# Kernel optimization log

Hardware: AMD Instinct MI355X
Metric: run time of the kernel (lower is better)

Reference implementation:

```python
import jax, jax.numpy as jnp
import numpy as np

B, N, PS = 8, 2048, 32
P = N // PS          # 64 patches
D, MLP, DEPTH, H, DH = 1024, 2048, 6, 8, 64
INNER = H * DH       # 512
K = 20
EPS = 1e-5


def setup_inputs() -> dict:
    key = jax.random.key(0)
    ks = jax.random.split(key, 16)
    r = lambda i, shape: jax.random.normal(ks[i], shape, dtype=jnp.float32) * 0.02
    return {
        "x": jax.random.normal(ks[0], (B, N, 3), dtype=jnp.float32),
        "x_pos_embed": r(1, (B, P + 1, D)),
        "w1": r(2, (64, 6)),   "g1": jnp.ones(64),  "b1": jnp.zeros(64),
        "w2": r(3, (64, 128)), "g2": jnp.ones(64),  "b2": jnp.zeros(64),
        "w3": r(4, (128, 128)),"g3": jnp.ones(128), "b3": jnp.zeros(128),
        "w4": r(5, (256, 256)),"g4": jnp.ones(256), "b4": jnp.zeros(256),
        "w5": r(6, (D, 512)),  "g5": jnp.ones(D),   "b5": jnp.zeros(D),
        "cls_token": r(7, (1, 1, D)),
        "ln1_g": jnp.ones((DEPTH, D)), "ln1_b": jnp.zeros((DEPTH, D)),
        "wqkv": r(8, (DEPTH, D, 3 * INNER)),
        "wout": r(9, (DEPTH, INNER, D)), "bout": jnp.zeros((DEPTH, D)),
        "ln2_g": jnp.ones((DEPTH, D)), "ln2_b": jnp.zeros((DEPTH, D)),
        "wff1": r(10, (DEPTH, D, MLP)), "bff1": jnp.zeros((DEPTH, MLP)),
        "wff2": r(11, (DEPTH, MLP, D)), "bff2": jnp.zeros((DEPTH, D)),
    }


def _knn(x, k):  # x: [B, C, N] -> neighbor idx [B, N, k]
    xx = jnp.sum(x * x, axis=1)                        # [B, N]
    inner = jnp.einsum('bcn,bcm->bnm', x, x)           # [B, N, N]
    dist = 2.0 * inner - xx[:, :, None] - xx[:, None, :]  # = -||xi-xj||^2
    return jax.lax.top_k(dist, k)[1]


def _graph_feature(x, k):  # x: [B, C, N] -> [B, N, k, 2C]
    idx = _knn(x, k)
    xt = jnp.transpose(x, (0, 2, 1))                   # [B, N, C]
    nbr = jax.vmap(lambda f, i: f[i])(xt, idx)         # gather: [B, N, k, C]
    ctr = jnp.broadcast_to(xt[:, :, None, :], nbr.shape)
    return jnp.concatenate([nbr - ctr, ctr], axis=-1)


def _leaky(v):
    return jnp.where(v >= 0, v, 0.2 * v)


def _edge_conv(x, w, g, b, k):  # EdgeConv block: graph feat -> 1x1 conv -> BN(train) -> lrelu -> max over k
    f = _graph_feature(x, k)                           # [B, N, k, 2C]
    y = jnp.einsum('bnkc,oc->bonk', f, w)              # [B, O, N, k]
    mu = jnp.mean(y, axis=(0, 2, 3), keepdims=True)
    var = jnp.var(y, axis=(0, 2, 3), keepdims=True)
    y = (y - mu) * jax.lax.rsqrt(var + EPS) * g[None, :, None, None] + b[None, :, None, None]
    return jnp.max(_leaky(y), axis=-1)                 # [B, O, N]


def _ln(x, g, b):
    mu = jnp.mean(x, axis=-1, keepdims=True)
    var = jnp.var(x, axis=-1, keepdims=True)
    return (x - mu) * jax.lax.rsqrt(var + EPS) * g + b


def reference(x, x_pos_embed, w1, g1, b1, w2, g2, b2, w3, g3, b3, w4, g4, b4,
              w5, g5, b5, cls_token, ln1_g, ln1_b, wqkv, wout, bout,
              ln2_g, ln2_b, wff1, bff1, wff2, bff2):
    scale = DH ** -0.5
    pts = jnp.transpose(x, (0, 2, 1))                  # [B, 3, N]
    x1 = _edge_conv(pts, w1, g1, b1, K)                # [B, 64, N]
    x2 = _edge_conv(x1, w2, g2, b2, K)                 # [B, 64, N]
    x3 = _edge_conv(x2, w3, g3, b3, K)                 # [B, 128, N]
    x4 = _edge_conv(x3, w4, g4, b4, K)                 # [B, 256, N]
    h = jnp.concatenate([x1, x2, x3, x4], axis=1)      # [B, 512, N]
    y = jnp.einsum('bcn,oc->bon', h, w5)               # conv5 1x1 -> [B, D, N]
    mu = jnp.mean(y, axis=(0, 2), keepdims=True)
    var = jnp.var(y, axis=(0, 2), keepdims=True)
    y = _leaky((y - mu) * jax.lax.rsqrt(var + EPS) * g5[None, :, None] + b5[None, :, None])
    # patch max-pool: 'b (p n) c -> (b p) n c' then max over n
    t = jnp.transpose(y, (0, 2, 1)).reshape(B * P, PS, D)
    t = jnp.max(t, axis=1).reshape(B, P, D)
    t = jnp.concatenate([jnp.broadcast_to(cls_token, (B, 1, D)), t], axis=1)  # [B, P+1, D]
    for i in range(DEPTH):
        t = t + x_pos_embed
        hn = _ln(t, ln1_g[i], ln1_b[i])
        qkv = (hn @ wqkv[i]).reshape(B, P + 1, 3, H, DH)
        q, k_, v = [jnp.transpose(qkv[:, :, j], (0, 2, 1, 3)) for j in range(3)]
        attn = jax.nn.softmax(jnp.einsum('bhld,bhmd->bhlm', q, k_) * scale, axis=-1)
        z = jnp.einsum('bhlm,bhmd->bhld', attn, v)
        z = jnp.transpose(z, (0, 2, 1, 3)).reshape(B, P + 1, INNER)
        t = t + z @ wout[i] + bout[i]
        hn = _ln(t, ln2_g[i], ln2_b[i])
        t = t + jax.nn.gelu(hn @ wff1[i] + bff1[i], approximate=False) @ wff2[i] + bff2[i]
    return t[:, 1:]                                    # [B, P, D]
```

## Files before the change

kernel.cpp:

```cpp
#include <hip/hip_runtime.h>
#include <math.h>

#define BB 8
#define NN 2048
#define PSZ 32
#define PP 64
#define DD 1024
#define MLPD 2048
#define DEPTH_ 6
#define HH 8
#define DHH 64
#define INNER_ 512
#define KK 20
#define TOK 65
#define EPSF 1e-5f

#define GEMM_ACC 1
#define GEMM_GELU 2
#define GEMM_OUTBF16 4

typedef __bf16 bf16_t;
typedef __attribute__((ext_vector_type(8))) __bf16 bf16x8;
typedef __attribute__((ext_vector_type(4))) float f32x4;

__global__ void transpose_x_kernel(const float* __restrict__ x, float* __restrict__ pts) {
    int gid = blockIdx.x * blockDim.x + threadIdx.x;
    if (gid >= BB * NN * 3) return;
    int c = gid % 3; int n = (gid / 3) % NN; int b = gid / (3 * NN);
    pts[(b * 3 + c) * NN + n] = x[gid];
}

__global__ void sqnorm_kernel(const float* __restrict__ x, int bs, int C, float* __restrict__ xx) {
    int gid = blockIdx.x * blockDim.x + threadIdx.x;
    if (gid >= BB * NN) return;
    int n = gid % NN; int b = gid / NN;
    const float* xp = x + b * bs + n;
    float s = 0.f;
    for (int c = 0; c < C; ++c) { float v = xp[c * NN]; s += v * v; }
    xx[gid] = s;
}

__global__ __launch_bounds__(256) void dist_kernel(const float* __restrict__ x, int bs, int C,
                                                   const float* __restrict__ xx, int b0,
                                                   float* __restrict__ dist) {
    __shared__ __align__(16) float smem[4224];
    float (*As)[132] = (float(*)[132])smem;
    float (*Bs)[132] = (float(*)[132])(smem + 16 * 132);
    float (*tb)[132] = (float(*)[132])smem;

    int q = blockIdx.x;
    int bi = 0, rem = q;
    while (rem >= (16 - bi)) { rem -= (16 - bi); ++bi; }
    int bj = bi + rem;

    int b = b0 + blockIdx.z;
    int n0 = bi * 128, m0 = bj * 128;
    int tid = threadIdx.x;
    int ty = tid >> 4, tx = tid & 15;
    float acc[2][2][4][4] = {};
    const float* xb = x + (long)b * bs;
    for (int k0 = 0; k0 < C; k0 += 16) {
        #pragma unroll
        for (int p = 0; p < 2; ++p) {
            int li = tid + p * 256;
            int i4 = li & 31;
            int kk = li >> 5;
            int c = k0 + kk;
            float4 va = make_float4(0.f, 0.f, 0.f, 0.f);
            float4 vb = va;
            if (c < C) {
                va = *(const float4*)&xb[(long)c * NN + n0 + i4 * 4];
                vb = *(const float4*)&xb[(long)c * NN + m0 + i4 * 4];
            }
            *(float4*)&As[kk][i4 * 4] = va;
            *(float4*)&Bs[kk][i4 * 4] = vb;
        }
        __syncthreads();
        #pragma unroll
        for (int kk = 0; kk < 16; ++kk) {
            float a[2][4], bv[2][4];
            *(float4*)a[0] = *(const float4*)&As[kk][ty * 4];
            *(float4*)a[1] = *(const float4*)&As[kk][64 + ty * 4];
            *(float4*)bv[0] = *(const float4*)&Bs[kk][tx * 4];
            *(float4*)bv[1] = *(const float4*)&Bs[kk][64 + tx * 4];
            #pragma unroll
            for (int ri = 0; ri < 2; ++ri)
                #pragma unroll
                for (int ci = 0; ci < 2; ++ci)
                    #pragma unroll
                    for (int i = 0; i < 4; ++i)
                        #pragma unroll
                        for (int j = 0; j < 4; ++j)
                            acc[ri][ci][i][j] += a[ri][i] * bv[ci][j];
        }
        __syncthreads();
    }
    float* db = dist + (long)blockIdx.z * NN * NN;
    const float* xxb = xx + b * NN;
    float xm[2][4];
    #pragma unroll
    for (int ci = 0; ci < 2; ++ci)
        #pragma unroll
        for (int j = 0; j < 4; ++j)
            xm[ci][j] = xxb[m0 + ci * 64 + tx * 4 + j];
    #pragma unroll
    for (int ri = 0; ri < 2; ++ri)
        #pragma unroll
        for (int i = 0; i < 4; ++i) {
            float xn = xxb[n0 + ri * 64 + ty * 4 + i];
            #pragma unroll
            for (int ci = 0; ci < 2; ++ci)
                #pragma unroll
                for (int j = 0; j < 4; ++j)
                    acc[ri][ci][i][j] = 2.f * acc[ri][ci][i][j] - xn - xm[ci][j];
        }
    #pragma unroll
    for (int ri = 0; ri < 2; ++ri)
        #pragma unroll
        for (int i = 0; i < 4; ++i) {
            int n = n0 + ri * 64 + ty * 4 + i;
            #pragma unroll
            for (int ci = 0; ci < 2; ++ci)
                *(float4*)&db[(long)n * NN + m0 + ci * 64 + tx * 4] = *(float4*)&acc[ri][ci][i][0];
        }
    if (bi != bj) {
        #pragma unroll
        for (int s = 0; s < 4; ++s) {
            __syncthreads();
            int ci = s >> 1;
            if ((tx >> 3) == (s & 1)) {
                #pragma unroll
                for (int ri = 0; ri < 2; ++ri)
                    #pragma unroll
                    for (int j = 0; j < 4; ++j) {
                        float4 v;
                        v.x = acc[ri][ci][0][j];
                        v.y = acc[ri][ci][1][j];
                        v.z = acc[ri][ci][2][j];
                        v.w = acc[ri][ci][3][j];
                        *(float4*)&tb[(tx & 7) * 4 + j][ri * 64 + ty * 4] = v;
                    }
            }
            __syncthreads();
            int r = tid >> 3;
            int c0 = (tid & 7) * 16;
            long orow = (long)(m0 + s * 32 + r) * NN + n0 + c0;
            #pragma unroll
            for (int c4 = 0; c4 < 4; ++c4)
                *(float4*)&db[orow + c4 * 4] = *(const float4*)&tb[r][c0 + c4 * 4];
        }
    }
}

__global__ __launch_bounds__(256) void topk_kernel(const float* __restrict__ dist, int b0,
                                                   int* __restrict__ idx) {
    __shared__ float cval[4][64];
    __shared__ int   cidx[4][64];
    int b = b0 + blockIdx.y;
    int wid = threadIdx.x >> 6, lane = threadIdx.x & 63;
    int n = blockIdx.x * 4 + wid;
    const float* row = dist + ((long)blockIdx.y * NN + n) * NN;
    float vals[32];
    #pragma unroll
    for (int s = 0; s < 32; ++s) vals[s] = row[s * 64 + lane];
    int* op = idx + ((long)b * NN + n) * KK;

    float lm = vals[0];
    #pragma unroll
    for (int s = 1; s < 32; ++s) lm = fmaxf(lm, vals[s]);

    float sv = lm;
    #pragma unroll
    for (int k = 2; k <= 64; k <<= 1) {
        #pragma unroll
        for (int j = k >> 1; j > 0; j >>= 1) {
            float pv = __shfl_xor(sv, j);
            bool lower = (lane & j) == 0;
            bool up = (lane & k) != 0;
            bool ownBetter = sv > pv;
            bool keepOwn = ownBetter ^ (lower == up);
            sv = keepOwn ? sv : pv;
        }
    }
    float t = __shfl(sv, 19);

    int base = 0;
    #pragma unroll
    for (int s = 0; s < 32; ++s) {
        bool q = vals[s] >= t;
        unsigned long long m = __ballot(q);
        int my = base + (int)__builtin_amdgcn_mbcnt_hi((unsigned)(m >> 32),
                         __builtin_amdgcn_mbcnt_lo((unsigned)m, 0u));
        if (q && my < 64) { cval[wid][my] = vals[s]; cidx[wid][my] = s * 64 + lane; }
        base += (int)__popcll(m);
    }
    __asm__ volatile("s_waitcnt lgkmcnt(0)" ::: "memory");

    if (base <= 64) {
        float v = (lane < base) ? cval[wid][lane] : -INFINITY;
        int   ii = (lane < base) ? cidx[wid][lane] : 0x7FFFFFFF;
        #pragma unroll
        for (int k = 2; k <= 64; k <<= 1) {
            #pragma unroll
            for (int j = k >> 1; j > 0; j >>= 1) {
                float pv = __shfl_xor(v, j);
                int   pi = __shfl_xor(ii, j);
                bool lower = (lane & j) == 0;
                bool up = (lane & k) != 0;
                bool ownBetter = (v > pv) || (v == pv && ii < pi);
                bool keepOwn = ownBetter ^ (lower == up);
                if (!keepOwn) { v = pv; ii = pi; }
            }
        }
        if (lane < KK) op[lane] = ii;
    } else {
        for (int kk = 0; kk < KK; ++kk) {
            float bv = vals[0]; int bsl = 0;
            #pragma unroll
            for (int s = 1; s < 32; ++s) if (vals[s] > bv) { bv = vals[s]; bsl = s; }
            int bm = bsl * 64 + lane;
            for (int off = 32; off; off >>= 1) {
                float ov = __shfl_xor(bv, off);
                int om = __shfl_xor(bm, off);
                if (ov > bv || (ov == bv && om < bm)) { bv = ov; bm = om; }
            }
            int wslot = bm >> 6, wlane = bm & 63;
            #pragma unroll
            for (int s = 0; s < 32; ++s)
                if (s == wslot) vals[s] = (lane == wlane) ? -INFINITY : vals[s];
            if (lane == 0) op[kk] = bm;
        }
    }
}

__global__ __launch_bounds__(256) void pq_kernel(const float* __restrict__ x, int bs, int C,
                                                 const float* __restrict__ w, int O,
                                                 float* __restrict__ p, float* __restrict__ q) {
    __shared__ float wT[256][33];
    __shared__ float xs[128][32];
    int b = blockIdx.z;
    int o0 = blockIdx.y * 32;
    int n0 = blockIdx.x * 32;
    int tid = threadIdx.x;
    for (int i = tid; i < 2 * C * 32; i += 256) {
        int c2 = i % (2 * C), o = i / (2 * C);
        wT[c2][o] = w[(o0 + o) * 2 * C + c2];
    }
    for (int i = tid; i < C * 32; i += 256) {
        int nl = i % 32, c = i / 32;
        xs[c][nl] = x[b * bs + c * NN + n0 + nl];
    }
    __syncthreads();
    int o_l = tid & 31;
    int n_base = (tid >> 5) * 4;
    float ps[4] = {0.f, 0.f, 0.f, 0.f};
    float qs[4] = {0.f, 0.f, 0.f, 0.f};
    for (int c = 0; c < C; ++c) {
        float4 xv = *(const float4*)&xs[c][n_base];
        float wa = wT[c][o_l];
        float wb = wT[C + c][o_l];
        float d = wb - wa;
        ps[0] += xv.x * wa; qs[0] += xv.x * d;
        ps[1] += xv.y * wa; qs[1] += xv.y * d;
        ps[2] += xv.z * wa; qs[2] += xv.z * d;
        ps[3] += xv.w * wa; qs[3] += xv.w * d;
    }
    for (int j = 0; j < 4; ++j) {
        long r = (long)(b * NN + n0 + n_base + j) * O + o0 + o_l;
        p[r] = ps[j];
        q[r] = qs[j];
    }
}

__global__ void zero_stats_kernel(double* __restrict__ s1, double* __restrict__ s2) {
    int t = blockIdx.x * blockDim.x + threadIdx.x;
    if (t < 1024) { s1[t] = 0.0; s2[t] = 0.0; }
}

__global__ __launch_bounds__(256) void edge_stats_kernel(const float* __restrict__ p, const float* __restrict__ q,
                                                         const int* __restrict__ idx, int O,
                                                         double* __restrict__ gsum, double* __restrict__ gsumsq) {
    int tid = threadIdx.x;
    int o = tid % O;
    int grp = tid / O;
    int ngrp = 256 / O;
    int rows_per_blk = (BB * NN) / gridDim.x;
    int r0 = blockIdx.x * rows_per_blk;
    double s = 0.0, ss = 0.0;
    for (int r = r0 + grp; r < r0 + rows_per_blk; r += ngrp) {
        int b = r / NN;
        float qv = q[r * O + o];
        for (int k = 0; k < KK; ++k) {
            int j = idx[r * KK + k];
            float v = p[(b * NN + j) * O + o] + qv;
            s += v; ss += (double)v * v;
        }
    }
    atomicAdd(&gsum[o], s);
    atomicAdd(&gsumsq[o], ss);
}

__global__ void bn_finalize_kernel(const double* __restrict__ gsum, const double* __restrict__ gsumsq,
                                   const float* __restrict__ g, const float* __restrict__ bb, int O, double cnt,
                                   float* __restrict__ scale, float* __restrict__ shift) {
    int o = blockIdx.x * blockDim.x + threadIdx.x;
    if (o >= O) return;
    double mean = gsum[o] / cnt;
    double var = gsumsq[o] / cnt - mean * mean;
    float inv = rsqrtf((float)var + EPSF);
    float sc = g[o] * inv;
    scale[o] = sc;
    shift[o] = bb[o] - (float)mean * sc;
}

__global__ void edge_out_kernel(const float* __restrict__ p, const float* __restrict__ q,
                                const int* __restrict__ idx, int O,
                                const float* __restrict__ scale, const float* __restrict__ shift,
                                float* __restrict__ out, int obs) {
    int gid = blockIdx.x * blockDim.x + threadIdx.x;
    if (gid >= BB * NN * O) return;
    int o = gid % O; int n = (gid / O) % NN; int b = gid / (O * NN);
    int r = b * NN + n;
    float qv = q[r * O + o];
    float sc = scale[o], sh = shift[o];
    float m = -INFINITY;
    for (int k = 0; k < KK; ++k) {
        int j = idx[r * KK + k];
        float v = (p[(b * NN + j) * O + o] + qv) * sc + sh;
        v = (v >= 0.f) ? v : 0.2f * v;
        m = fmaxf(m, v);
    }
    out[b * obs + o * NN + n] = m;
}

__global__ __launch_bounds__(256) void transpose_cvt_kernel(const float* __restrict__ in,
                                                            bf16_t* __restrict__ outp,
                                                            int R, int C, long s_in, long s_out) {
    __shared__ float tile[32][33];
    const float* ib = in + (long)blockIdx.z * s_in;
    bf16_t* ob = outp + (long)blockIdx.z * s_out;
    int r0 = blockIdx.y * 32, c0 = blockIdx.x * 32;
    int tx = threadIdx.x & 31, tg = threadIdx.x >> 5;
    for (int i = 0; i < 4; ++i) {
        int r = tg + i * 8;
        tile[r][tx] = ib[(long)(r0 + r) * C + c0 + tx];
    }
    __syncthreads();
    for (int i = 0; i < 4; ++i) {
        int c = tg + i * 8;
        ob[(long)(c0 + c) * R + r0 + tx] = (bf16_t)tile[tx][c];
    }
}

__global__ __launch_bounds__(256) void gemm_bf16_kernel(const float* __restrict__ A,
                                                        const bf16_t* __restrict__ Bt,
                                                        const float* __restrict__ bias,
                                                        float* __restrict__ out,
                                                        int M, int Kd, int Nd,
                                                        long sA, long sBt, long sO, int flags) {
    __shared__ __align__(16) bf16_t As[64 * 32];
    __shared__ __align__(16) bf16_t Bs[64 * 32];
    const float* Ab = A + (long)blockIdx.z * sA;
    const bf16_t* Bb = Bt + (long)blockIdx.z * sBt;
    int row0 = blockIdx.y * 64, col0 = blockIdx.x * 64;
    int tid = threadIdx.x;
    int lane = tid & 63, wv = tid >> 6;
    int wm = wv >> 1, wn = wv & 1;
    int srow = tid >> 2;
    int skp = (tid & 3) * 8;
    f32x4 acc[2][2] = {};
    for (int k0 = 0; k0 < Kd; k0 += 32) {
        {
            int r = row0 + srow;
            float av[8];
            if (r < M) {
                const float* ap = Ab + (long)r * Kd + k0 + skp;
                float4 a0 = *(const float4*)ap;
                float4 a1 = *(const float4*)(ap + 4);
                av[0] = a0.x; av[1] = a0.y; av[2] = a0.z; av[3] = a0.w;
                av[4] = a1.x; av[5] = a1.y; av[6] = a1.z; av[7] = a1.w;
            } else {
                #pragma unroll
                for (int j = 0; j < 8; ++j) av[j] = 0.f;
            }
            bf16x8 v;
            #pragma unroll
            for (int j = 0; j < 8; ++j) v[j] = (bf16_t)av[j];
            *(bf16x8*)&As[((skp >> 3) * 64 + srow) * 8] = v;
        }
        {
            const bf16_t* bp = Bb + (long)(col0 + srow) * Kd + k0 + skp;
            bf16x8 v = *(const bf16x8*)bp;
            *(bf16x8*)&Bs[((skp >> 3) * 64 + srow) * 8] = v;
        }
        __syncthreads();
        int q = lane >> 4, cl = lane & 15;
        bf16x8 a0v = *(const bf16x8*)&As[(q * 64 + wm * 32 + cl) * 8];
        bf16x8 a1v = *(const bf16x8*)&As[(q * 64 + wm * 32 + 16 + cl) * 8];
        bf16x8 b0v = *(const bf16x8*)&Bs[(q * 64 + wn * 32 + cl) * 8];
        bf16x8 b1v = *(const bf16x8*)&Bs[(q * 64 + wn * 32 + 16 + cl) * 8];
        acc[0][0] = __builtin_amdgcn_mfma_f32_16x16x32_bf16(a0v, b0v, acc[0][0], 0, 0, 0);
        acc[0][1] = __builtin_amdgcn_mfma_f32_16x16x32_bf16(a0v, b1v, acc[0][1], 0, 0, 0);
        acc[1][0] = __builtin_amdgcn_mfma_f32_16x16x32_bf16(a1v, b0v, acc[1][0], 0, 0, 0);
        acc[1][1] = __builtin_amdgcn_mfma_f32_16x16x32_bf16(a1v, b1v, acc[1][1], 0, 0, 0);
        __syncthreads();
    }
    int q = lane >> 4, cl = lane & 15;
    float* Obf = out + (long)blockIdx.z * sO;
    bf16_t* Obh = (bf16_t*)out + (long)blockIdx.z * sO;
    for (int mt = 0; mt < 2; ++mt)
        for (int nt = 0; nt < 2; ++nt)
            #pragma unroll
            for (int r = 0; r < 4; ++r) {
                int row = row0 + wm * 32 + mt * 16 + q * 4 + r;
                if (row >= M) continue;
                int col = col0 + wn * 32 + nt * 16 + cl;
                float v = acc[mt][nt][r];
                if (bias) v += bias[col];
                if (flags & GEMM_GELU) v = 0.5f * v * (1.f + erff(v * 0.70710678118654752f));
                long oidx = (long)row * Nd + col;
                if (flags & GEMM_OUTBF16) Obh[oidx] = (bf16_t)v;
                else if (flags & GEMM_ACC) Obf[oidx] += v;
                else Obf[oidx] = v;
            }
}

__global__ __launch_bounds__(256) void gemm_kernel(const float* __restrict__ A, const float* __restrict__ Bm,
                                                   const float* __restrict__ bias, float* __restrict__ out,
                                                   int M, int Kd, int Nd, long sA, long sB, long sO, int flags) {
    __shared__ float As[16][65];
    __shared__ float Bs[16][64];
    const float* Ab = A + (long)blockIdx.z * sA;
    const float* Bb = Bm + (long)blockIdx.z * sB;
    float* Ob = out + (long)blockIdx.z * sO;
    int row0 = blockIdx.y * 64, col0 = blockIdx.x * 64;
    int tid = threadIdx.x;
    int ty = tid / 16, tx = tid % 16;
    float acc[4][4] = {};
    for (int k0 = 0; k0 < Kd; k0 += 16) {
        for (int i = 0; i < 4; ++i) {
            int li = tid + i * 256;
            int m = li / 16, kk = li % 16;
            int r = row0 + m;
            As[kk][m] = (r < M) ? Ab[(long)r * Kd + k0 + kk] : 0.f;
        }
        for (int i = 0; i < 4; ++i) {
            int li = tid + i * 256;
            int kk = li / 64, n = li % 64;
            int c = col0 + n;
            Bs[kk][n] = (c < Nd) ? Bb[(long)(k0 + kk) * Nd + c] : 0.f;
        }
        __syncthreads();
        for (int kk = 0; kk < 16; ++kk) {
            float a[4], bv[4];
            for (int i = 0; i < 4; ++i) a[i] = As[kk][ty * 4 + i];
            for (int j = 0; j < 4; ++j) bv[j] = Bs[kk][tx * 4 + j];
            for (int i = 0; i < 4; ++i)
                for (int j = 0; j < 4; ++j)
                    acc[i][j] += a[i] * bv[j];
        }
        __syncthreads();
    }
    for (int i = 0; i < 4; ++i) {
        int r = row0 + ty * 4 + i;
        if (r >= M) continue;
        for (int j = 0; j < 4; ++j) {
            int c = col0 + tx * 4 + j;
            if (c >= Nd) continue;
            float v = acc[i][j];
            if (bias) v += bias[c];
            if (flags & GEMM_GELU) v = 0.5f * v * (1.f + erff(v * 0.70710678118654752f));
            long oidx = (long)r * Nd + c;
            if (flags & GEMM_ACC) Ob[oidx] += v; else Ob[oidx] = v;
        }
    }
}

__global__ __launch_bounds__(256) void bn5_stats_bf16_kernel(const bf16_t* __restrict__ y5,
                                                             const float* __restrict__ g,
                                                             const float* __restrict__ bb,
                                                             float* __restrict__ scale, float* __restrict__ shift) {
    __shared__ double ssum[256], ssq[256];
    int d = blockIdx.x;
    int tid = threadIdx.x;
    double s = 0.0, sq = 0.0;
    for (int b = 0; b < BB; ++b) {
        const bf16_t* row = y5 + ((long)b * DD + d) * NN;
        for (int n = tid; n < NN; n += 256) { float v = (float)row[n]; s += v; sq += (double)v * v; }
    }
    ssum[tid] = s; ssq[tid] = sq;
    __syncthreads();
    for (int st = 128; st > 0; st >>= 1) {
        if (tid < st) { ssum[tid] += ssum[tid + st]; ssq[tid] += ssq[tid + st]; }
        __syncthreads();
    }
    if (tid == 0) {
        double cnt = (double)BB * NN;
        double mean = ssum[0] / cnt;
        double var = ssq[0] / cnt - mean * mean;
        float inv = rsqrtf((float)var + EPSF);
        float sc = g[d] * inv;
        scale[d] = sc;
        shift[d] = bb[d] - (float)mean * sc;
    }
}

__global__ __launch_bounds__(256) void bn5_stats_kernel(const float* __restrict__ y5, const float* __restrict__ g,
                                                        const float* __restrict__ bb,
                                                        float* __restrict__ scale, float* __restrict__ shift) {
    __shared__ double ssum[256], ssq[256];
    int d = blockIdx.x;
    int tid = threadIdx.x;
    double s = 0.0, sq = 0.0;
    for (int b = 0; b < BB; ++b) {
        const float* row = y5 + ((long)b * DD + d) * NN;
        for (int n = tid; n < NN; n += 256) { float v = row[n]; s += v; sq += (double)v * v; }
    }
    ssum[tid] = s; ssq[tid] = sq;
    __syncthreads();
    for (int st = 128; st > 0; st >>= 1) {
        if (tid < st) { ssum[tid] += ssum[tid + st]; ssq[tid] += ssq[tid + st]; }
        __syncthreads();
    }
    if (tid == 0) {
        double cnt = (double)BB * NN;
        double mean = ssum[0] / cnt;
        double var = ssq[0] / cnt - mean * mean;
        float inv = rsqrtf((float)var + EPSF);
        float sc = g[d] * inv;
        scale[d] = sc;
        shift[d] = bb[d] - (float)mean * sc;
    }
}

__global__ void pool_bf16_kernel(const bf16_t* __restrict__ y5, const float* __restrict__ scale,
                                 const float* __restrict__ shift, const float* __restrict__ cls,
                                 float* __restrict__ t) {
    int gid = blockIdx.x * blockDim.x + threadIdx.x;
    if (gid >= BB * TOK * DD) return;
    int d = gid % DD; int l = (gid / DD) % TOK; int b = gid / (DD * TOK);
    float v;
    if (l == 0) {
        v = cls[d];
    } else {
        int pp = l - 1;
        const bf16_t* row = y5 + ((long)b * DD + d) * NN + pp * PSZ;
        float sc = scale[d], sh = shift[d];
        float m = -INFINITY;
        for (int i = 0; i < PSZ; ++i) {
            float u = (float)row[i] * sc + sh;
            u = (u >= 0.f) ? u : 0.2f * u;
            m = fmaxf(m, u);
        }
        v = m;
    }
    t[gid] = v;
}

__global__ void pool_kernel(const float* __restrict__ y5, const float* __restrict__ scale,
                            const float* __restrict__ shift, const float* __restrict__ cls,
                            float* __restrict__ t) {
    int gid = blockIdx.x * blockDim.x + threadIdx.x;
    if (gid >= BB * TOK * DD) return;
    int d = gid % DD; int l = (gid / DD) % TOK; int b = gid / (DD * TOK);
    float v;
    if (l == 0) {
        v = cls[d];
    } else {
        int pp = l - 1;
        const float* row = y5 + ((long)b * DD + d) * NN + pp * PSZ;
        float sc = scale[d], sh = shift[d];
        float m = -INFINITY;
        for (int i = 0; i < PSZ; ++i) {
            float u = row[i] * sc + sh;
            u = (u >= 0.f) ? u : 0.2f * u;
            m = fmaxf(m, u);
        }
        v = m;
    }
    t[gid] = v;
}

__global__ __launch_bounds__(256) void ln_kernel(float* __restrict__ t, const float* __restrict__ pos,
                                                 const float* __restrict__ g, const float* __restrict__ bb,
                                                 float* __restrict__ hn, int addpos) {
    __shared__ double s1[256], s2[256];
    long r = blockIdx.x;
    int tid = threadIdx.x;
    float vals[4];
    double s = 0.0, sq = 0.0;
    for (int i = 0; i < 4; ++i) {
        int d = tid + i * 256;
        float v = t[r * DD + d];
        if (addpos) { v += pos[r * DD + d]; t[r * DD + d] = v; }
        vals[i] = v; s += v; sq += (double)v * v;
    }
    s1[tid] = s; s2[tid] = sq;
    __syncthreads();
    for (int st = 128; st > 0; st >>= 1) {
        if (tid < st) { s1[tid] += s1[tid + st]; s2[tid] += s2[tid + st]; }
        __syncthreads();
    }
    double mean = s1[0] / DD;
    float var = (float)(s2[0] / DD - mean * mean);
    float fm = (float)mean;
    float inv = rsqrtf(var + EPSF);
    for (int i = 0; i < 4; ++i) {
        int d = tid + i * 256;
        hn[r * DD + d] = (vals[i] - fm) * inv * g[d] + bb[d];
    }
}

__global__ __launch_bounds__(256) void attn_kernel(const float* __restrict__ qkv, float* __restrict__ z) {
    __shared__ float ks[TOK][DHH + 1];
    __shared__ float vs[TOK][DHH + 1];
    __shared__ float ss[TOK][TOK];
    int bh = blockIdx.x;
    int b = bh / HH, h = bh % HH;
    int tid = threadIdx.x;
    for (int i = tid; i < TOK * DHH; i += 256) {
        int l = i / DHH, d = i % DHH;
        long base = (long)(b * TOK + l) * 1536;
        ks[l][d] = qkv[base + 512 + h * DHH + d];
        vs[l][d] = qkv[base + 1024 + h * DHH + d];
    }
    __syncthreads();
    for (int i = tid; i < TOK * TOK; i += 256) {
        int l = i / TOK, m = i % TOK;
        const float* qrow = qkv + (long)(b * TOK + l) * 1536 + h * DHH;
        float acc = 0.f;
        for (int d = 0; d < DHH; ++d) acc += qrow[d] * ks[m][d];
        ss[l][m] = acc * 0.125f;
    }
    __syncthreads();
    if (tid < TOK) {
        float mx = -INFINITY;
        for (int m = 0; m < TOK; ++m) mx = fmaxf(mx, ss[tid][m]);
        float sum = 0.f;
        for (int m = 0; m < TOK; ++m) { float e = expf(ss[tid][m] - mx); ss[tid][m] = e; sum += e; }
        float invs = 1.f / sum;
        for (int m = 0; m < TOK; ++m) ss[tid][m] *= invs;
    }
    __syncthreads();
    for (int i = tid; i < TOK * DHH; i += 256) {
        int l = i / DHH, d = i % DHH;
        float acc = 0.f;
        for (int m = 0; m < TOK; ++m) acc += ss[l][m] * vs[m][d];
        z[(long)(b * TOK + l) * INNER_ + h * DHH + d] = acc;
    }
}

__global__ void final_kernel(const float* __restrict__ t, float* __restrict__ out) {
    int gid = blockIdx.x * blockDim.x + threadIdx.x;
    if (gid >= BB * PP * DD) return;
    int d = gid % DD; int p = (gid / DD) % PP; int b = gid / (DD * PP);
    out[gid] = t[((long)b * TOK + 1 + p) * DD + d];
}

static inline int ceil_div(long a, long b) { return (int)((a + b - 1) / b); }

extern "C" void kernel_launch(void* const* d_in, const int* in_sizes, int n_in,
                              void* d_out, int out_size, void* d_ws, size_t ws_size,
                              hipStream_t stream) {
    const float* x    = (const float*)d_in[0];
    const float* pos  = (const float*)d_in[1];
    const float* w1   = (const float*)d_in[2];
    const float* g1   = (const float*)d_in[3];
    const float* b1   = (const float*)d_in[4];
    const float* w2   = (const float*)d_in[5];
    const float* g2   = (const float*)d_in[6];
    const float* b2   = (const float*)d_in[7];
    const float* w3   = (const float*)d_in[8];
    const float* g3   = (const float*)d_in[9];
    const float* b3   = (const float*)d_in[10];
    const float* w4   = (const float*)d_in[11];
    const float* g4   = (const float*)d_in[12];
    const float* b4   = (const float*)d_in[13];
    const float* w5   = (const float*)d_in[14];
    const float* g5   = (const float*)d_in[15];
    const float* b5   = (const float*)d_in[16];
    const float* cls  = (const float*)d_in[17];
    const float* ln1g = (const float*)d_in[18];
    const float* ln1b = (const float*)d_in[19];
    const float* wqkv = (const float*)d_in[20];
    const float* wout = (const float*)d_in[21];
    const float* bout = (const float*)d_in[22];
    const float* ln2g = (const float*)d_in[23];
    const float* ln2b = (const float*)d_in[24];
    const float* wff1 = (const float*)d_in[25];
    const float* bff1 = (const float*)d_in[26];
    const float* wff2 = (const float*)d_in[27];
    const float* bff2 = (const float*)d_in[28];
    float* out = (float*)d_out;

    char* ws = (char*)d_ws;
    size_t off = 0;
    auto alloc = [&](size_t bytes) -> char* {
        char* ptr = ws + off;
        off = (off + bytes + 255) & ~(size_t)255;
        return ptr;
    };
    float*  h      = (float*)alloc((size_t)BB * 512 * NN * 4);
    float*  t      = (float*)alloc((size_t)BB * TOK * DD * 4);
    float*  hn     = (float*)alloc((size_t)BB * TOK * DD * 4);
    float*  qkvb   = (float*)alloc((size_t)BB * TOK * 1536 * 4);
    float*  zb     = (float*)alloc((size_t)BB * TOK * INNER_ * 4);
    float*  ub     = (float*)alloc((size_t)BB * TOK * MLPD * 4);
    double* dsum   = (double*)alloc(1024 * 8);
    double* dsq    = (double*)alloc(1024 * 8);
    float*  scaleb = (float*)alloc(1024 * 4);
    float*  shiftb = (float*)alloc(1024 * 4);
    size_t ubase = off;

    size_t uoff = ubase;
    auto ualloc = [&](size_t bytes) -> char* {
        char* ptr = ws + uoff;
        uoff = (uoff + bytes + 255) & ~(size_t)255;
        return ptr;
    };
    float* pts  = (float*)ualloc((size_t)BB * 3 * NN * 4);
    float* xx   = (float*)ualloc((size_t)BB * NN * 4);
    int*   idxb = (int*)  ualloc((size_t)BB * NN * KK * 4);
    float* pbuf = (float*)ualloc((size_t)BB * NN * 256 * 4);
    float* qbuf = (float*)ualloc((size_t)BB * NN * 256 * 4);
    size_t dist_rel = uoff - ubase;
    float* distb = (float*)(ws + uoff);

    size_t voff = ubase;
    auto valloc = [&](size_t bytes) -> char* {
        char* ptr = ws + voff;
        voff = (voff + bytes + 255) & ~(size_t)255;
        return ptr;
    };
    bf16_t* hT     = (bf16_t*)valloc((size_t)BB * NN * 512 * 2);
    bf16_t* wTqkv  = (bf16_t*)valloc((size_t)DEPTH_ * 1536 * DD * 2);
    bf16_t* wTout  = (bf16_t*)valloc((size_t)DEPTH_ * DD * INNER_ * 2);
    bf16_t* wTff1  = (bf16_t*)valloc((size_t)DEPTH_ * MLPD * DD * 2);
    bf16_t* wTff2  = (bf16_t*)valloc((size_t)DEPTH_ * DD * MLPD * 2);
    size_t stage_bf16 = voff - ubase;

    size_t conv_full  = dist_rel + (size_t)BB * NN * NN * 4;
    size_t conv_batch = dist_rel + (size_t)NN * NN * 4;
    size_t stage_fp32 = (size_t)BB * DD * NN * 4;

    auto mx = [](size_t a, size_t b) { return a > b ? a : b; };
    bool use_bf16 = ws_size >= ubase + mx(conv_batch, stage_bf16);
    bool full     = ws_size >= ubase + mx(conv_full, use_bf16 ? stage_bf16 : stage_fp32);
    if (!use_bf16 && ws_size < ubase + mx(conv_batch, stage_fp32)) return;
    bf16_t* y5bf = (bf16_t*)h;
    float*  y5f  = (float*)(ws + ubase);

    transpose_x_kernel<<<ceil_div((long)BB * NN * 3, 256), 256, 0, stream>>>(x, pts);

    const int NTRI = 136;
    auto run_conv = [&](const float* xin, int xbs, int C, const float* w,
                        const float* g, const float* bb, float* hout, int O) {
        sqnorm_kernel<<<ceil_div((long)BB * NN, 256), 256, 0, stream>>>(xin, xbs, C, xx);
        if (full) {
            dist_kernel<<<dim3(NTRI, 1, BB), 256, 0, stream>>>(xin, xbs, C, xx, 0, distb);
            topk_kernel<<<dim3(NN / 4, BB), 256, 0, stream>>>(distb, 0, idxb);
        } else {
            for (int b = 0; b < BB; ++b) {
                dist_kernel<<<dim3(NTRI, 1, 1), 256, 0, stream>>>(xin, xbs, C, xx, b, distb);
                topk_kernel<<<dim3(NN / 4, 1), 256, 0, stream>>>(distb, b, idxb);
            }
        }
        {
            dim3 grid(NN / 32, O / 32, BB);
            pq_kernel<<<grid, 256, 0, stream>>>(xin, xbs, C, w, O, pbuf, qbuf);
        }
        zero_stats_kernel<<<4, 256, 0, stream>>>(dsum, dsq);
        edge_stats_kernel<<<256, 256, 0, stream>>>(pbuf, qbuf, idxb, O, dsum, dsq);
        bn_finalize_kernel<<<1, 256, 0, stream>>>(dsum, dsq, g, bb, O, (double)BB * NN * KK, scaleb, shiftb);
        edge_out_kernel<<<ceil_div((long)BB * NN * O, 256), 256, 0, stream>>>(
            pbuf, qbuf, idxb, O, scaleb, shiftb, hout, 512 * NN);
    };
    run_conv(pts, 3 * NN, 3, w1, g1, b1, h, 64);
    run_conv(h, 512 * NN, 64, w2, g2, b2, h + 64 * NN, 64);
    run_conv(h + 64 * NN, 512 * NN, 64, w3, g3, b3, h + 128 * NN, 128);
    run_conv(h + 128 * NN, 512 * NN, 128, w4, g4, b4, h + 256 * NN, 256);

    const int M = BB * TOK;
    if (use_bf16) {
        transpose_cvt_kernel<<<dim3(NN / 32, 512 / 32, BB), 256, 0, stream>>>(
            h, hT, 512, NN, (long)512 * NN, (long)NN * 512);
        transpose_cvt_kernel<<<dim3(1536 / 32, DD / 32, DEPTH_), 256, 0, stream>>>(
            wqkv, wTqkv, DD, 1536, (long)DD * 1536, (long)1536 * DD);
        transpose_cvt_kernel<<<dim3(DD / 32, INNER_ / 32, DEPTH_), 256, 0, stream>>>(
            wout, wTout, INNER_, DD, (long)INNER_ * DD, (long)DD * INNER_);
        transpose_cvt_kernel<<<dim3(MLPD / 32, DD / 32, DEPTH_), 256, 0, stream>>>(
            wff1, wTff1, DD, MLPD, (long)DD * MLPD, (long)MLPD * DD);
        transpose_cvt_kernel<<<dim3(DD / 32, MLPD / 32, DEPTH_), 256, 0, stream>>>(
            wff2, wTff2, MLPD, DD, (long)MLPD * DD, (long)DD * MLPD);

        gemm_bf16_kernel<<<dim3(NN / 64, DD / 64, BB), 256, 0, stream>>>(
            w5, hT, nullptr, (float*)y5bf, DD, 512, NN, 0L, (long)NN * 512, (long)DD * NN, GEMM_OUTBF16);
        bn5_stats_bf16_kernel<<<DD, 256, 0, stream>>>(y5bf, g5, b5, scaleb, shiftb);
        pool_bf16_kernel<<<ceil_div((long)BB * TOK * DD, 256), 256, 0, stream>>>(y5bf, scaleb, shiftb, cls, t);

        for (int i = 0; i < DEPTH_; ++i) {
            ln_kernel<<<M, 256, 0, stream>>>(t, pos, ln1g + i * DD, ln1b + i * DD, hn, 1);
            gemm_bf16_kernel<<<dim3(1536 / 64, ceil_div(M, 64), 1), 256, 0, stream>>>(
                hn, wTqkv + (size_t)i * 1536 * DD, nullptr, qkvb, M, DD, 1536, 0L, 0L, 0L, 0);
            attn_kernel<<<BB * HH, 256, 0, stream>>>(qkvb, zb);
            gemm_bf16_kernel<<<dim3(DD / 64, ceil_div(M, 64), 1), 256, 0, stream>>>(
                zb, wTout + (size_t)i * DD * INNER_, bout + i * DD, t, M, INNER_, DD, 0L, 0L, 0L, GEMM_ACC);
            ln_kernel<<<M, 256, 0, stream>>>(t, nullptr, ln2g + i * DD, ln2b + i * DD, hn, 0);
            gemm_bf16_kernel<<<dim3(MLPD / 64, ceil_div(M, 64), 1), 256, 0, stream>>>(
                hn, wTff1 + (size_t)i * MLPD * DD, bff1 + i * MLPD, ub, M, DD, MLPD, 0L, 0L, 0L, GEMM_GELU);
            gemm_bf16_kernel<<<dim3(DD / 64, ceil_div(M, 64), 1), 256, 0, stream>>>(
                ub, wTff2 + (size_t)i * DD * MLPD, bff2 + i * DD, t, M, MLPD, DD, 0L, 0L, 0L, GEMM_ACC);
        }
    } else {
        gemm_kernel<<<dim3(NN / 64, DD / 64, BB), 256, 0, stream>>>(
            w5, h, nullptr, y5f, DD, 512, NN, 0L, (long)512 * NN, (long)DD * NN, 0);
        bn5_stats_kernel<<<DD, 256, 0, stream>>>(y5f, g5, b5, scaleb, shiftb);
        pool_kernel<<<ceil_div((long)BB * TOK * DD, 256), 256, 0, stream>>>(y5f, scaleb, shiftb, cls, t);
        for (int i = 0; i < DEPTH_; ++i) {
            ln_kernel<<<M, 256, 0, stream>>>(t, pos, ln1g + i * DD, ln1b + i * DD, hn, 1);
            gemm_kernel<<<dim3(1536 / 64, ceil_div(M, 64), 1), 256, 0, stream>>>(
                hn, wqkv + (size_t)i * DD * 1536, nullptr, qkvb, M, DD, 1536, 0L, 0L, 0L, 0);
            attn_kernel<<<BB * HH, 256, 0, stream>>>(qkvb, zb);
            gemm_kernel<<<dim3(DD / 64, ceil_div(M, 64), 1), 256, 0, stream>>>(
                zb, wout + (size_t)i * INNER_ * DD, bout + i * DD, t, M, INNER_, DD, 0L, 0L, 0L, GEMM_ACC);
            ln_kernel<<<M, 256, 0, stream>>>(t, nullptr, ln2g + i * DD, ln2b + i * DD, hn, 0);
            gemm_kernel<<<dim3(MLPD / 64, ceil_div(M, 64), 1), 256, 0, stream>>>(
                hn, wff1 + (size_t)i * DD * MLPD, bff1 + i * MLPD, ub, M, DD, MLPD, 0L, 0L, 0L, GEMM_GELU);
            gemm_kernel<<<dim3(DD / 64, ceil_div(M, 64), 1), 256, 0, stream>>>(
                ub, wff2 + (size_t)i * MLPD * DD, bff2 + i * DD, t, M, MLPD, DD, 0L, 0L, 0L, GEMM_ACC);
        }
    }

    final_kernel<<<ceil_div((long)BB * PP * DD, 256), 256, 0, stream>>>(t, out);
}
```

Baseline: 2.018 ms.

## Use bf16 activations and async global-to-LDS loads in the bf16 GEMM

```diff
diff --git a/kernel.cpp b/kernel.cpp
--- a/kernel.cpp
+++ b/kernel.cpp
@@ -22,6 +22,13 @@
 typedef __bf16 bf16_t;
 typedef __attribute__((ext_vector_type(8))) __bf16 bf16x8;
 typedef __attribute__((ext_vector_type(4))) float f32x4;
+
+__device__ __forceinline__ void async_copy16(const bf16_t* gsrc, bf16_t* ldst) {
+    __builtin_amdgcn_global_load_lds(
+        (const __attribute__((address_space(1))) unsigned int*)gsrc,
+        (__attribute__((address_space(3))) unsigned int*)ldst,
+        16, 0, 0);
+}
 
 __global__ void transpose_x_kernel(const float* __restrict__ x, float* __restrict__ pts) {
     int gid = blockIdx.x * blockDim.x + threadIdx.x;
@@ -352,7 +359,18 @@
     }
 }
 
-__global__ __launch_bounds__(256) void gemm_bf16_kernel(const float* __restrict__ A,
+__global__ void cvt_bf16_kernel(const float* __restrict__ in, bf16_t* __restrict__ outp, long n8) {
+    long g = (long)blockIdx.x * blockDim.x + threadIdx.x;
+    if (g >= n8) return;
+    const float4* pp = (const float4*)(in + g * 8);
+    float4 a = pp[0], b = pp[1];
+    bf16x8 v;
+    v[0] = (bf16_t)a.x; v[1] = (bf16_t)a.y; v[2] = (bf16_t)a.z; v[3] = (bf16_t)a.w;
+    v[4] = (bf16_t)b.x; v[5] = (bf16_t)b.y; v[6] = (bf16_t)b.z; v[7] = (bf16_t)b.w;
+    *(bf16x8*)(outp + g * 8) = v;
+}
+
+__global__ __launch_bounds__(256) void gemm_bf16_kernel(const bf16_t* __restrict__ A,
                                                         const bf16_t* __restrict__ Bt,
                                                         const float* __restrict__ bias,
                                                         float* __restrict__ out,
@@ -360,39 +378,22 @@
                                                         long sA, long sBt, long sO, int flags) {
     __shared__ __align__(16) bf16_t As[64 * 32];
     __shared__ __align__(16) bf16_t Bs[64 * 32];
-    const float* Ab = A + (long)blockIdx.z * sA;
+    const bf16_t* Ab = A + (long)blockIdx.z * sA;
     const bf16_t* Bb = Bt + (long)blockIdx.z * sBt;
     int row0 = blockIdx.y * 64, col0 = blockIdx.x * 64;
     int tid = threadIdx.x;
     int lane = tid & 63, wv = tid >> 6;
     int wm = wv >> 1, wn = wv & 1;
-    int srow = tid >> 2;
-    int skp = (tid & 3) * 8;
+    int srow = tid & 63;
+    int sk = wv * 8;
+    const bf16_t* ap = Ab + (long)(row0 + srow) * Kd + sk;
+    const bf16_t* bp = Bb + (long)(col0 + srow) * Kd + sk;
+    bf16_t* lA = &As[wv * 512];
+    bf16_t* lB = &Bs[wv * 512];
     f32x4 acc[2][2] = {};
     for (int k0 = 0; k0 < Kd; k0 += 32) {
-        {
-            int r = row0 + srow;
-            float av[8];
-            if (r < M) {
-                const float* ap = Ab + (long)r * Kd + k0 + skp;
-                float4 a0 = *(const float4*)ap;
-                float4 a1 = *(const float4*)(ap + 4);
-                av[0] = a0.x; av[1] = a0.y; av[2] = a0.z; av[3] = a0.w;
-                av[4] = a1.x; av[5] = a1.y; av[6] = a1.z; av[7] = a1.w;
-            } else {
-                #pragma unroll
-                for (int j = 0; j < 8; ++j) av[j] = 0.f;
-            }
-            bf16x8 v;
-            #pragma unroll
-            for (int j = 0; j < 8; ++j) v[j] = (bf16_t)av[j];
-            *(bf16x8*)&As[((skp >> 3) * 64 + srow) * 8] = v;
-        }
-        {
-            const bf16_t* bp = Bb + (long)(col0 + srow) * Kd + k0 + skp;
-            bf16x8 v = *(const bf16x8*)bp;
-            *(bf16x8*)&Bs[((skp >> 3) * 64 + srow) * 8] = v;
-        }
+        async_copy16(ap + k0, lA);
+        async_copy16(bp + k0, lB);
         __syncthreads();
         int q = lane >> 4, cl = lane & 15;
         bf16x8 a0v = *(const bf16x8*)&As[(q * 64 + wm * 32 + cl) * 8];
@@ -425,57 +426,6 @@
             }
 }
 
-__global__ __launch_bounds__(256) void gemm_kernel(const float* __restrict__ A, const float* __restrict__ Bm,
-                                                   const float* __restrict__ bias, float* __restrict__ out,
-                                                   int M, int Kd, int Nd, long sA, long sB, long sO, int flags) {
-    __shared__ float As[16][65];
-    __shared__ float Bs[16][64];
-    const float* Ab = A + (long)blockIdx.z * sA;
-    const float* Bb = Bm + (long)blockIdx.z * sB;
-    float* Ob = out + (long)blockIdx.z * sO;
-    int row0 = blockIdx.y * 64, col0 = blockIdx.x * 64;
-    int tid = threadIdx.x;
-    int ty = tid / 16, tx = tid % 16;
-    float acc[4][4] = {};
-    for (int k0 = 0; k0 < Kd; k0 += 16) {
-        for (int i = 0; i < 4; ++i) {
-            int li = tid + i * 256;
-            int m = li / 16, kk = li % 16;
-            int r = row0 + m;
-            As[kk][m] = (r < M) ? Ab[(long)r * Kd + k0 + kk] : 0.f;
-        }
-        for (int i = 0; i < 4; ++i) {
-            int li = tid + i * 256;
-            int kk = li / 64, n = li % 64;
-            int c = col0 + n;
-            Bs[kk][n] = (c < Nd) ? Bb[(long)(k0 + kk) * Nd + c] : 0.f;
-        }
-        __syncthreads();
-        for (int kk = 0; kk < 16; ++kk) {
-            float a[4], bv[4];
-            for (int i = 0; i < 4; ++i) a[i] = As[kk][ty * 4 + i];
-            for (int j = 0; j < 4; ++j) bv[j] = Bs[kk][tx * 4 + j];
-            for (int i = 0; i < 4; ++i)
-                for (int j = 0; j < 4; ++j)
-                    acc[i][j] += a[i] * bv[j];
-        }
-        __syncthreads();
-    }
-    for (int i = 0; i < 4; ++i) {
-        int r = row0 + ty * 4 + i;
-        if (r >= M) continue;
-        for (int j = 0; j < 4; ++j) {
-            int c = col0 + tx * 4 + j;
-            if (c >= Nd) continue;
-            float v = acc[i][j];
-            if (bias) v += bias[c];
-            if (flags & GEMM_GELU) v = 0.5f * v * (1.f + erff(v * 0.70710678118654752f));
-            long oidx = (long)r * Nd + c;
-            if (flags & GEMM_ACC) Ob[oidx] += v; else Ob[oidx] = v;
-        }
-    }
-}
-
 __global__ __launch_bounds__(256) void bn5_stats_bf16_kernel(const bf16_t* __restrict__ y5,
                                                              const float* __restrict__ g,
                                                              const float* __restrict__ bb,
@@ -487,34 +437,6 @@
     for (int b = 0; b < BB; ++b) {
         const bf16_t* row = y5 + ((long)b * DD + d) * NN;
         for (int n = tid; n < NN; n += 256) { float v = (float)row[n]; s += v; sq += (double)v * v; }
-    }
-    ssum[tid] = s; ssq[tid] = sq;
-    __syncthreads();
-    for (int st = 128; st > 0; st >>= 1) {
-        if (tid < st) { ssum[tid] += ssum[tid + st]; ssq[tid] += ssq[tid + st]; }
-        __syncthreads();
-    }
-    if (tid == 0) {
-        double cnt = (double)BB * NN;
-        double mean = ssum[0] / cnt;
-        double var = ssq[0] / cnt - mean * mean;
-        float inv = rsqrtf((float)var + EPSF);
-        float sc = g[d] * inv;
-        scale[d] = sc;
-        shift[d] = bb[d] - (float)mean * sc;
-    }
-}
-
-__global__ __launch_bounds__(256) void bn5_stats_kernel(const float* __restrict__ y5, const float* __restrict__ g,
-                                                        const float* __restrict__ bb,
-                                                        float* __restrict__ scale, float* __restrict__ shift) {
-    __shared__ double ssum[256], ssq[256];
-    int d = blockIdx.x;
-    int tid = threadIdx.x;
-    double s = 0.0, sq = 0.0;
-    for (int b = 0; b < BB; ++b) {
-        const float* row = y5 + ((long)b * DD + d) * NN;
-        for (int n = tid; n < NN; n += 256) { float v = row[n]; s += v; sq += (double)v * v; }
     }
     ssum[tid] = s; ssq[tid] = sq;
     __syncthreads();
@@ -557,33 +479,9 @@
     t[gid] = v;
 }
 
-__global__ void pool_kernel(const float* __restrict__ y5, const float* __restrict__ scale,
-                            const float* __restrict__ shift, const float* __restrict__ cls,
-                            float* __restrict__ t) {
-    int gid = blockIdx.x * blockDim.x + threadIdx.x;
-    if (gid >= BB * TOK * DD) return;
-    int d = gid % DD; int l = (gid / DD) % TOK; int b = gid / (DD * TOK);
-    float v;
-    if (l == 0) {
-        v = cls[d];
-    } else {
-        int pp = l - 1;
-        const float* row = y5 + ((long)b * DD + d) * NN + pp * PSZ;
-        float sc = scale[d], sh = shift[d];
-        float m = -INFINITY;
-        for (int i = 0; i < PSZ; ++i) {
-            float u = row[i] * sc + sh;
-            u = (u >= 0.f) ? u : 0.2f * u;
-            m = fmaxf(m, u);
-        }
-        v = m;
-    }
-    t[gid] = v;
-}
-
 __global__ __launch_bounds__(256) void ln_kernel(float* __restrict__ t, const float* __restrict__ pos,
                                                  const float* __restrict__ g, const float* __restrict__ bb,
-                                                 float* __restrict__ hn, int addpos) {
+                                                 bf16_t* __restrict__ hn, int addpos) {
     __shared__ double s1[256], s2[256];
     long r = blockIdx.x;
     int tid = threadIdx.x;
@@ -607,11 +505,11 @@
     float inv = rsqrtf(var + EPSF);
     for (int i = 0; i < 4; ++i) {
         int d = tid + i * 256;
-        hn[r * DD + d] = (vals[i] - fm) * inv * g[d] + bb[d];
-    }
-}
-
-__global__ __launch_bounds__(256) void attn_kernel(const float* __restrict__ qkv, float* __restrict__ z) {
+        hn[r * DD + d] = (bf16_t)((vals[i] - fm) * inv * g[d] + bb[d]);
+    }
+}
+
+__global__ __launch_bounds__(256) void attn_kernel(const float* __restrict__ qkv, bf16_t* __restrict__ z) {
     __shared__ float ks[TOK][DHH + 1];
     __shared__ float vs[TOK][DHH + 1];
     __shared__ float ss[TOK][TOK];
@@ -646,7 +544,7 @@
         int l = i / DHH, d = i % DHH;
         float acc = 0.f;
         for (int m = 0; m < TOK; ++m) acc += ss[l][m] * vs[m][d];
-        z[(long)(b * TOK + l) * INNER_ + h * DHH + d] = acc;
+        z[(long)(b * TOK + l) * INNER_ + h * DHH + d] = (bf16_t)acc;
     }
 }
 
@@ -702,10 +600,10 @@
     };
     float*  h      = (float*)alloc((size_t)BB * 512 * NN * 4);
     float*  t      = (float*)alloc((size_t)BB * TOK * DD * 4);
-    float*  hn     = (float*)alloc((size_t)BB * TOK * DD * 4);
+    bf16_t* hnb    = (bf16_t*)alloc((size_t)BB * TOK * DD * 4);
     float*  qkvb   = (float*)alloc((size_t)BB * TOK * 1536 * 4);
-    float*  zb     = (float*)alloc((size_t)BB * TOK * INNER_ * 4);
-    float*  ub     = (float*)alloc((size_t)BB * TOK * MLPD * 4);
+    bf16_t* zbb    = (bf16_t*)alloc((size_t)BB * TOK * INNER_ * 4);
+    bf16_t* ubb    = (bf16_t*)alloc((size_t)BB * TOK * MLPD * 4);
     double* dsum   = (double*)alloc(1024 * 8);
     double* dsq    = (double*)alloc(1024 * 8);
     float*  scaleb = (float*)alloc(1024 * 4);
@@ -737,18 +635,17 @@
     bf16_t* wTout  = (bf16_t*)valloc((size_t)DEPTH_ * DD * INNER_ * 2);
     bf16_t* wTff1  = (bf16_t*)valloc((size_t)DEPTH_ * MLPD * DD * 2);
     bf16_t* wTff2  = (bf16_t*)valloc((size_t)DEPTH_ * DD * MLPD * 2);
+    bf16_t* w5b    = (bf16_t*)valloc((size_t)DD * 512 * 2);
     size_t stage_bf16 = voff - ubase;
 
     size_t conv_full  = dist_rel + (size_t)BB * NN * NN * 4;
     size_t conv_batch = dist_rel + (size_t)NN * NN * 4;
-    size_t stage_fp32 = (size_t)BB * DD * NN * 4;
 
     auto mx = [](size_t a, size_t b) { return a > b ? a : b; };
     bool use_bf16 = ws_size >= ubase + mx(conv_batch, stage_bf16);
-    bool full     = ws_size >= ubase + mx(conv_full, use_bf16 ? stage_bf16 : stage_fp32);
-    if (!use_bf16 && ws_size < ubase + mx(conv_batch, stage_fp32)) return;
+    bool full     = ws_size >= ubase + mx(conv_full, stage_bf16);
+    if (!use_bf16) return;
     bf16_t* y5bf = (bf16_t*)h;
-    float*  y5f  = (float*)(ws + ubase);
 
     transpose_x_kernel<<<ceil_div((long)BB * NN * 3, 256), 256, 0, stream>>>(x, pts);
 
@@ -781,54 +678,37 @@
     run_conv(h + 128 * NN, 512 * NN, 128, w4, g4, b4, h + 256 * NN, 256);
 
     const int M = BB * TOK;
-    if (use_bf16) {
-        transpose_cvt_kernel<<<dim3(NN / 32, 512 / 32, BB), 256, 0, stream>>>(
-            h, hT, 512, NN, (long)512 * NN, (long)NN * 512);
-        transpose_cvt_kernel<<<dim3(1536 / 32, DD / 32, DEPTH_), 256, 0, stream>>>(
-            wqkv, wTqkv, DD, 1536, (long)DD * 1536, (long)1536 * DD);
-        transpose_cvt_kernel<<<dim3(DD / 32, INNER_ / 32, DEPTH_), 256, 0, stream>>>(
-            wout, wTout, INNER_, DD, (long)INNER_ * DD, (long)DD * INNER_);
-        transpose_cvt_kernel<<<dim3(MLPD / 32, DD / 32, DEPTH_), 256, 0, stream>>>(
-            wff1, wTff1, DD, MLPD, (long)DD * MLPD, (long)MLPD * DD);
-        transpose_cvt_kernel<<<dim3(DD / 32, MLPD / 32, DEPTH_), 256, 0, stream>>>(
-            wff2, wTff2, MLPD, DD, (long)MLPD * DD, (long)DD * MLPD);
-
-        gemm_bf16_kernel<<<dim3(NN / 64, DD / 64, BB), 256, 0, stream>>>(
-            w5, hT, nullptr, (float*)y5bf, DD, 512, NN, 0L, (long)NN * 512, (long)DD * NN, GEMM_OUTBF16);
-        bn5_stats_bf16_kernel<<<DD, 256, 0, stream>>>(y5bf, g5, b5, scaleb, shiftb);
-        pool_bf16_kernel<<<ceil_div((long)BB * TOK * DD, 256), 256, 0, stream>>>(y5bf, scaleb, shiftb, cls, t);
-
-        for (int i = 0; i < DEPTH_; ++i) {
-            ln_kernel<<<M, 256, 0, stream>>>(t, pos, ln1g + i * DD, ln1b + i * DD, hn, 1);
-            gemm_bf16_kernel<<<dim3(1536 / 64, ceil_div(M, 64), 1), 256, 0, stream>>>(
-                hn, wTqkv + (size_t)i * 1536 * DD, nullptr, qkvb, M, DD, 1536, 0L, 0L, 0L, 0);
-            attn_kernel<<<BB * HH, 256, 0, stream>>>(qkvb, zb);
-            gemm_bf16_kernel<<<dim3(DD / 64, ceil_div(M, 64), 1), 256, 0, stream>>>(
-                zb, wTout + (size_t)i * DD * INNER_, bout + i * DD, t, M, INNER_, DD, 0L, 0L, 0L, GEMM_ACC);
-            ln_kernel<<<M, 256, 0, stream>>>(t, nullptr, ln2g + i * DD, ln2b + i * DD, hn, 0);
-            gemm_bf16_kernel<<<dim3(MLPD / 64, ceil_div(M, 64), 1), 256, 0, stream>>>(
-                hn, wTff1 + (size_t)i * MLPD * DD, bff1 + i * MLPD, ub, M, DD, MLPD, 0L, 0L, 0L, GEMM_GELU);
-            gemm_bf16_kernel<<<dim3(DD / 64, ceil_div(M, 64), 1), 256, 0, stream>>>(
-                ub, wTff2 + (size_t)i * DD * MLPD, bff2 + i * DD, t, M, MLPD, DD, 0L, 0L, 0L, GEMM_ACC);
-        }
-    } else {
-        gemm_kernel<<<dim3(NN / 64, DD / 64, BB), 256, 0, stream>>>(
-            w5, h, nullptr, y5f, DD, 512, NN, 0L, (long)512 * NN, (long)DD * NN, 0);
-        bn5_stats_kernel<<<DD, 256, 0, stream>>>(y5f, g5, b5, scaleb, shiftb);
-        pool_kernel<<<ceil_div((long)BB * TOK * DD, 256), 256, 0, stream>>>(y5f, scaleb, shiftb, cls, t);
-        for (int i = 0; i < DEPTH_; ++i) {
-            ln_kernel<<<M, 256, 0, stream>>>(t, pos, ln1g + i * DD, ln1b + i * DD, hn, 1);
-            gemm_kernel<<<dim3(1536 / 64, ceil_div(M, 64), 1), 256, 0, stream>>>(
-                hn, wqkv + (size_t)i * DD * 1536, nullptr, qkvb, M, DD, 1536, 0L, 0L, 0L, 0);
-            attn_kernel<<<BB * HH, 256, 0, stream>>>(qkvb, zb);
-            gemm_kernel<<<dim3(DD / 64, ceil_div(M, 64), 1), 256, 0, stream>>>(
-                zb, wout + (size_t)i * INNER_ * DD, bout + i * DD, t, M, INNER_, DD, 0L, 0L, 0L, GEMM_ACC);
-            ln_kernel<<<M, 256, 0, stream>>>(t, nullptr, ln2g + i * DD, ln2b + i * DD, hn, 0);
-            gemm_kernel<<<dim3(MLPD / 64, ceil_div(M, 64), 1), 256, 0, stream>>>(
-                hn, wff1 + (size_t)i * DD * MLPD, bff1 + i * MLPD, ub, M, DD, MLPD, 0L, 0L, 0L, GEMM_GELU);
-            gemm_kernel<<<dim3(DD / 64, ceil_div(M, 64), 1), 256, 0, stream>>>(
-                ub, wff2 + (size_t)i * MLPD * DD, bff2 + i * DD, t, M, MLPD, DD, 0L, 0L, 0L, GEMM_ACC);
-        }
+
+    transpose_cvt_kernel<<<dim3(NN / 32, 512 / 32, BB), 256, 0, stream>>>(
+        h, hT, 512, NN, (long)512 * NN, (long)NN * 512);
+    transpose_cvt_kernel<<<dim3(1536 / 32, DD / 32, DEPTH_), 256, 0, stream>>>(
+        wqkv, wTqkv, DD, 1536, (long)DD * 1536, (long)1536 * DD);
+    transpose_cvt_kernel<<<dim3(DD / 32, INNER_ / 32, DEPTH_), 256, 0, stream>>>(
+        wout, wTout, INNER_, DD, (long)INNER_ * DD, (long)DD * INNER_);
+    transpose_cvt_kernel<<<dim3(MLPD / 32, DD / 32, DEPTH_), 256, 0, stream>>>(
+        wff1, wTff1, DD, MLPD, (long)DD * MLPD, (long)MLPD * DD);
+    transpose_cvt_kernel<<<dim3(DD / 32, MLPD / 32, DEPTH_), 256, 0, stream>>>(
+        wff2, wTff2, MLPD, DD, (long)MLPD * DD, (long)DD * MLPD);
+    cvt_bf16_kernel<<<ceil_div((long)DD * 512 / 8, 256), 256, 0, stream>>>(w5, w5b, (long)DD * 512 / 8);
+
+    gemm_bf16_kernel<<<dim3(NN / 64, DD / 64, BB), 256, 0, stream>>>(
+        w5b, hT, nullptr, (float*)y5bf, DD, 512, NN, 0L, (long)NN * 512, (long)DD * NN, GEMM_OUTBF16);
+    bn5_stats_bf16_kernel<<<DD, 256, 0, stream>>>(y5bf, g5, b5, scaleb, shiftb);
+    pool_bf16_kernel<<<ceil_div((long)BB * TOK * DD, 256), 256, 0, stream>>>(y5bf, scaleb, shiftb, cls, t);
+
+    for (int i = 0; i < DEPTH_; ++i) {
+        ln_kernel<<<M, 256, 0, stream>>>(t, pos, ln1g + i * DD, ln1b + i * DD, hnb, 1);
+        gemm_bf16_kernel<<<dim3(1536 / 64, ceil_div(M, 64), 1), 256, 0, stream>>>(
+            hnb, wTqkv + (size_t)i * 1536 * DD, nullptr, qkvb, M, DD, 1536, 0L, 0L, 0L, 0);
+        attn_kernel<<<BB * HH, 256, 0, stream>>>(qkvb, zbb);
+        gemm_bf16_kernel<<<dim3(DD / 64, ceil_div(M, 64), 1), 256, 0, stream>>>(
+            zbb, wTout + (size_t)i * DD * INNER_, bout + i * DD, t, M, INNER_, DD, 0L, 0L, 0L, GEMM_ACC);
+        ln_kernel<<<M, 256, 0, stream>>>(t, nullptr, ln2g + i * DD, ln2b + i * DD, hnb, 0);
+        gemm_bf16_kernel<<<dim3(MLPD / 64, ceil_div(M, 64), 1), 256, 0, stream>>>(
+            hnb, wTff1 + (size_t)i * MLPD * DD, bff1 + i * MLPD, (float*)ubb, M, DD, MLPD,
+            0L, 0L, 0L, GEMM_GELU | GEMM_OUTBF16);
+        gemm_bf16_kernel<<<dim3(DD / 64, ceil_div(M, 64), 1), 256, 0, stream>>>(
+            ubb, wTff2 + (size_t)i * DD * MLPD, bff2 + i * DD, t, M, MLPD, DD, 0L, 0L, 0L, GEMM_ACC);
     }
 
     final_kernel<<<ceil_div((long)BB * PP * DD, 256), 256, 0, stream>>>(t, out);
```

Result: no change. 2.018 ms (-0.0%).
